# Kernel optimization log

Measured on AMD Instinct MI355X. Metric: run time of the kernel, lower is better.

## Reference

```python
import jax, jax.numpy as jnp
import numpy as np

B, V, F = 16384, 20, 15
H = 256

def setup_inputs() -> dict:
    key = jax.random.key(0)
    ks = jax.random.split(key, 16)
    s = 0.05  # small init scale to keep sigmoids/tanh unsaturated
    return {
        "state": jax.random.normal(ks[0], (B, V, F), jnp.float32),
        "W_ih": jax.random.normal(ks[1], (3 * H, F), jnp.float32) * s,
        "W_hh": jax.random.normal(ks[2], (3 * H, H), jnp.float32) * s,
        "b_ih": jax.random.normal(ks[3], (3 * H,), jnp.float32) * s,
        "b_hh": jax.random.normal(ks[4], (3 * H,), jnp.float32) * s,
        "W1": jax.random.normal(ks[5], (1024, H + F), jnp.float32) * s,
        "b1": jax.random.normal(ks[6], (1024,), jnp.float32) * s,
        "W2": jax.random.normal(ks[7], (1024, 1024), jnp.float32) * s,
        "b2": jax.random.normal(ks[8], (1024,), jnp.float32) * s,
        "W3": jax.random.normal(ks[9], (512, 1024), jnp.float32) * s,
        "b3": jax.random.normal(ks[10], (512,), jnp.float32) * s,
        "W4": jax.random.normal(ks[11], (256, 512), jnp.float32) * s,
        "b4": jax.random.normal(ks[12], (256,), jnp.float32) * s,
        "Wp": jax.random.normal(ks[13], (1, 256), jnp.float32) * s,
        "bp": jax.random.normal(ks[14], (1,), jnp.float32) * s,
    }

def reference(state, W_ih, W_hh, b_ih, b_hh, W1, b1, W2, b2, W3, b3, W4, b4, Wp, bp):
    # state: [B, V, F] -- V vehicles per timestep, F=15 features each.
    # Precompute input-side gate pre-activations for all vehicles: [B, V, 3H]
    xg = jnp.einsum('bvf,gf->bvg', state, W_ih) + b_ih
    h0 = jnp.zeros((state.shape[0], H), state.dtype)

    def gru_step(h, xg_t):  # xg_t: [B, 3H]
        hg = h @ W_hh.T + b_hh  # [B, 3H]
        xr, xz, xn = jnp.split(xg_t, 3, axis=-1)
        hr, hz, hn = jnp.split(hg, 3, axis=-1)
        r = jax.nn.sigmoid(xr + hr)
        z = jax.nn.sigmoid(xz + hz)
        n = jnp.tanh(xn + r * hn)
        return (1.0 - z) * n + z * h, None

    h, _ = jax.lax.scan(gru_step, h0, jnp.swapaxes(xg, 0, 1))  # scan over V
    x = jnp.concatenate([state[:, 0, :], h], axis=-1)  # [B, F+H]
    x = jax.nn.relu(x @ W1.T + b1)
    x = jax.nn.relu(x @ W2.T + b2)
    x = jax.nn.relu(x @ W3.T + b3)
    x = jax.nn.relu(x @ W4.T + b4)
    return jnp.tanh(x @ Wp.T + bp)  # [B, action_dim]
```

## Files before the change

kernel.cpp:

```cpp
#include <hip/hip_runtime.h>


typedef __attribute__((ext_vector_type(8))) __bf16 bf16x8;
typedef __attribute__((ext_vector_type(4))) __bf16 bf16x4;
typedef __attribute__((ext_vector_type(4))) float  floatx4;

#define MFMA16(a, b, c) __builtin_amdgcn_mfma_f32_16x16x32_bf16((a), (b), (c), 0, 0, 0)

#define GL_LDS16(g, l)                                                         \
    __builtin_amdgcn_global_load_lds(                                          \
        (const __attribute__((address_space(1))) void*)(g),                    \
        (__attribute__((address_space(3))) void*)(l), 16, 0, 0)

__device__ __forceinline__ float sigmoid_f(float x) { return 1.f / (1.f + __expf(-x)); }
__device__ __forceinline__ float tanh_f(float x)    { return 1.f - 2.f / (1.f + __expf(2.f * x)); }

#define S0 147456u
#define S1 442368u
#define S2 1490944u
#define S3 2015232u
#define S4 2146304u
#define S5 2154496u
#define S6 2220032u
#define S7 2220544u
#define S8 2221056u

__global__ void prep_kernel(const float* __restrict__ W_ih, const float* __restrict__ W_hh,
                            const float* __restrict__ b_ih, const float* __restrict__ b_hh,
                            const float* __restrict__ W1, const float* __restrict__ W2,
                            const float* __restrict__ W3, const float* __restrict__ W4,
                            __bf16* __restrict__ Wg1, __bf16* __restrict__ W1p,
                            __bf16* __restrict__ W2b, __bf16* __restrict__ W3b,
                            __bf16* __restrict__ W4b, __bf16* __restrict__ Win_n,
                            __bf16* __restrict__ Whh_n, float* __restrict__ bsum,
                            float* __restrict__ bihn, float* __restrict__ bhhn)
{
    for (unsigned i = blockIdx.x * blockDim.x + threadIdx.x; i < S8; i += gridDim.x * blockDim.x) {
        if (i < S0) {
            unsigned g = i / 288u, c = i % 288u;
            float v;
            if (c < 15u)       v = W_ih[g * 15u + c];
            else if (c == 15u) v = b_ih[g] + b_hh[g];
            else if (c < 32u)  v = 0.f;
            else               v = W_hh[g * 256u + (c - 32u)];
            Wg1[i] = (__bf16)v;
        } else if (i < S1) {
            unsigned t = i - S0, o = t / 288u, c = t % 288u;
            float v = (c < 15u) ? W1[o * 271u + c] : ((c < 32u) ? 0.f : W1[o * 271u + (c - 17u)]);
            W1p[t] = (__bf16)v;
        } else if (i < S2) {
            unsigned t = i - S1; W2b[t] = (__bf16)W2[t];
        } else if (i < S3) {
            unsigned t = i - S2; W3b[t] = (__bf16)W3[t];
        } else if (i < S4) {
            unsigned t = i - S3; W4b[t] = (__bf16)W4[t];
        } else if (i < S5) {
            unsigned t = i - S4, j = t / 32u, c = t % 32u;
            float v;
            if (c < 15u)       v = W_ih[(512u + j) * 15u + c];
            else if (c == 15u) v = b_ih[512u + j];
            else               v = 0.f;
            Win_n[t] = (__bf16)v;
        } else if (i < S6) {
            unsigned t = i - S5; Whh_n[t] = (__bf16)W_hh[512u * 256u + t];
        } else if (i < S7) {
            unsigned t = i - S6; bsum[t] = b_ih[t] + b_hh[t];
        } else {
            unsigned t = i - S7;
            if (t < 256u) bihn[t] = b_ih[512u + t];
            else          bhhn[t - 256u] = b_hh[512u + t - 256u];
        }
    }
}

#define HSTRIDE 264
#define HBUF_N  (64 * HSTRIDE)

__global__ __launch_bounds__(1024)
void gru_kernel(const float* __restrict__ state,
                const __bf16* __restrict__ Wg1,  const __bf16* __restrict__ Win_n,
                const __bf16* __restrict__ Whh_n,
                const float* __restrict__ bhhn, __bf16* __restrict__ x0)
{
    __shared__ __bf16 hbuf[2 * HBUF_N];
    __shared__ __bf16 sbuf[2 * 2048];
    __shared__ __bf16 rzbuf[4 * 1024 * 8];

    const int tid  = threadIdx.x;
    const int wave = tid >> 6;
    const int lane = tid & 63;
    const int q    = lane >> 4;
    const int ln   = lane & 15;
    const int b0   = blockIdx.x * 64;

    {
        bf16x8 z = {};
        bf16x8* p = (bf16x8*)hbuf;
        #pragma unroll 3
        for (int i = tid; i < HBUF_N / 8; i += 1024) p[i] = z;
        if (tid < 512) ((bf16x8*)sbuf)[tid] = z;
    }
    const int srow = tid >> 4, sk = tid & 15;

    const floatx4 Bhn = *(const floatx4*)(bhhn + wave * 16 + q * 4);

    const int jr = wave * 16 + ln;
    const __bf16* wr = Wg1   + (size_t)jr * 288 + q * 8;
    const __bf16* wz = Wg1   + (size_t)(256 + jr) * 288 + q * 8;
    const __bf16* wx = Win_n + (size_t)jr * 32  + q * 8;
    const __bf16* wh = Whh_n + (size_t)jr * 256 + q * 8;

    const __bf16* hread  = hbuf + ln * HSTRIDE + q * 8;
    __bf16*       hwrite = hbuf + ln * HSTRIDE + wave * 16 + q * 4;
    const __bf16* sread  = sbuf + ln * 32 + q * 8;
    __bf16*       rzw    = rzbuf + tid * 8;

    if (sk < 15)
        sbuf[srow * 32 + sk] = (__bf16)state[(size_t)(b0 + srow) * 300 + sk];
    if (tid < 128) sbuf[(tid >> 6) * 2048 + (tid & 63) * 32 + 15] = (__bf16)1.0f;
    __syncthreads();

#define GRU_STEP(v, SB)                                                          \
    {                                                                            \
        float snext = 0.f;                                                       \
        if ((v) < 19 && sk < 15)                                                 \
            snext = state[(size_t)(b0 + srow) * 300 + ((v) + 1) * 15 + sk];      \
        _Pragma("unroll 1")                                                      \
        for (int p = 0; p < 2; ++p) {                                            \
            floatx4 acc0[4], acc1[4];                                            \
            const floatx4 zf = {0.f, 0.f, 0.f, 0.f};                             \
            _Pragma("unroll")                                                    \
            for (int nt = 0; nt < 4; nt++) { acc0[nt] = zf; acc1[nt] = zf; }     \
            if (p == 0) {                                                        \
                {                                                                \
                    bf16x8 a0 = *(const bf16x8*)(wr);                            \
                    bf16x8 a1 = *(const bf16x8*)(wz);                            \
                    _Pragma("unroll")                                            \
                    for (int nt = 0; nt < 4; nt++) {                             \
                        bf16x8 b = *(const bf16x8*)(sread + (SB) * 2048 +        \
                                                    nt * 512);                   \
                        acc0[nt] = MFMA16(a0, b, acc0[nt]);                      \
                        acc1[nt] = MFMA16(a1, b, acc1[nt]);                      \
                    }                                                            \
                }                                                                \
                _Pragma("unroll")                                                \
                for (int kk = 0; kk < 8; ++kk) {                                 \
                    bf16x8 a0 = *(const bf16x8*)(wr + 32 + kk * 32);             \
                    bf16x8 a1 = *(const bf16x8*)(wz + 32 + kk * 32);             \
                    _Pragma("unroll")                                            \
                    for (int nt = 0; nt < 4; nt++) {                             \
                        bf16x8 b = *(const bf16x8*)(hread + (SB) * HBUF_N +      \
                                                    nt * (16 * HSTRIDE) +        \
                                                    kk * 32);                    \
                        acc0[nt] = MFMA16(a0, b, acc0[nt]);                      \
                        acc1[nt] = MFMA16(a1, b, acc1[nt]);                      \
                    }                                                            \
                }                                                                \
                _Pragma("unroll")                                                \
                for (int nt = 0; nt < 4; nt++) {                                 \
                    bf16x8 rz;                                                   \
                    _Pragma("unroll")                                            \
                    for (int r = 0; r < 4; r++) {                                \
                        rz[r]     = (__bf16)sigmoid_f(acc0[nt][r]);              \
                        rz[4 + r] = (__bf16)sigmoid_f(acc1[nt][r]);              \
                    }                                                            \
                    *(bf16x8*)(rzw + nt * 8192) = rz;                            \
                }                                                                \
            } else {                                                             \
                {                                                                \
                    bf16x8 a0 = *(const bf16x8*)(wx);                            \
                    _Pragma("unroll")                                            \
                    for (int nt = 0; nt < 4; nt++) {                             \
                        bf16x8 b = *(const bf16x8*)(sread + (SB) * 2048 +        \
                                                    nt * 512);                   \
                        acc0[nt] = MFMA16(a0, b, acc0[nt]);                      \
                    }                                                            \
                }                                                                \
                _Pragma("unroll")                                                \
                for (int kk = 0; kk < 8; ++kk) {                                 \
                    bf16x8 a1 = *(const bf16x8*)(wh + kk * 32);                  \
                    _Pragma("unroll")                                            \
                    for (int nt = 0; nt < 4; nt++) {                             \
                        bf16x8 b = *(const bf16x8*)(hread + (SB) * HBUF_N +      \
                                                    nt * (16 * HSTRIDE) +        \
                                                    kk * 32);                    \
                        acc1[nt] = MFMA16(a1, b, acc1[nt]);                      \
                    }                                                            \
                }                                                                \
                _Pragma("unroll")                                                \
                for (int nt = 0; nt < 4; nt++) {                                 \
                    bf16x8 rz = *(const bf16x8*)(rzw + nt * 8192);               \
                    bf16x4 ho = *(const bf16x4*)(hwrite + (SB) * HBUF_N +        \
                                                 nt * (16 * HSTRIDE));           \
                    bf16x4 hv;                                                   \
                    _Pragma("unroll")                                            \
                    for (int r = 0; r < 4; r++) {                                \
                        float rg = (float)rz[r];                                 \
                        float zg = (float)rz[4 + r];                             \
                        float nn = tanh_f(acc0[nt][r] +                          \
                                          rg * (acc1[nt][r] + Bhn[r]));          \
                        float hnew = (1.f - zg) * nn + zg * (float)ho[r];        \
                        hv[r] = (__bf16)hnew;                                    \
                    }                                                            \
                    *(bf16x4*)(hwrite + (1 - (SB)) * HBUF_N +                    \
                               nt * (16 * HSTRIDE)) = hv;                        \
                }                                                                \
            }                                                                    \
        }                                                                        \
        if ((v) < 19 && sk < 15)                                                 \
            sbuf[(1 - (SB)) * 2048 + srow * 32 + sk] = (__bf16)snext;            \
        __syncthreads();                                                         \
    }

    #pragma unroll 1
    for (int v2 = 0; v2 < 10; ++v2) {
        GRU_STEP(2 * v2,     0)
        GRU_STEP(2 * v2 + 1, 1)
    }
#undef GRU_STEP

    {
        const int row = tid >> 4, p = tid & 15;
        #pragma unroll
        for (int s = 0; s < 2; s++) {
            const int col = p * 8 + s * 128;
            *(bf16x8*)(x0 + (size_t)(b0 + row) * 288 + 32 + col) =
                *(const bf16x8*)(hbuf + row * HSTRIDE + col);
        }
    }
    #pragma unroll
    for (int t = 0; t < 2; t++) {
        int i = tid + t * 1024;
        int row = i >> 5, c = i & 31;
        float s = (c < 15) ? state[(size_t)(b0 + row) * 300 + c] : 0.f;
        x0[(size_t)(b0 + row) * 288 + c] = (__bf16)s;
    }
}

__global__ __launch_bounds__(256)
void gemm_bias_act(const __bf16* __restrict__ A, const __bf16* __restrict__ W,
                   const float* __restrict__ bias, __bf16* __restrict__ C,
                   int N, int K, int relu)
{
    __shared__ __bf16 smem[128 * 136];
    __bf16* At = smem;
    __bf16* Bt = smem + 4096;

    const int tid  = threadIdx.x;
    const int wave = tid >> 6, lane = tid & 63;
    const int q = lane >> 4, ln = lane & 15;
    const int wm = wave >> 1, wn = wave & 1;
    const int arow0 = blockIdx.x * 128;
    const int bcol0 = blockIdx.y * 128;

    float bv[4];
    #pragma unroll
    for (int n = 0; n < 4; n++) bv[n] = bias[bcol0 + wn * 64 + n * 16 + ln];

    floatx4 acc[4][4];
    const floatx4 zf = {0.f, 0.f, 0.f, 0.f};
    #pragma unroll
    for (int m = 0; m < 4; m++)
        #pragma unroll
        for (int n = 0; n < 4; n++) acc[m][n] = zf;

    const int stg_row = wave * 16 + (lane >> 2);
    const int stg_k   = (lane & 3) * 8;
    const int lds_off = wave * 512;

    for (int kt = 0; kt < K; kt += 32) {
        #pragma unroll
        for (int rd = 0; rd < 2; rd++) {
            GL_LDS16(A + (size_t)(arow0 + stg_row + rd * 64) * K + kt + stg_k,
                     At + lds_off + rd * 2048);
            GL_LDS16(W + (size_t)(bcol0 + stg_row + rd * 64) * K + kt + stg_k,
                     Bt + lds_off + rd * 2048);
        }
        __syncthreads();
        bf16x8 af[4], bf[4];
        #pragma unroll
        for (int m = 0; m < 4; m++)
            af[m] = *(const bf16x8*)(At + (wm * 64 + m * 16 + ln) * 32 + q * 8);
        #pragma unroll
        for (int n = 0; n < 4; n++)
            bf[n] = *(const bf16x8*)(Bt + (wn * 64 + n * 16 + ln) * 32 + q * 8);
        #pragma unroll
        for (int n = 0; n < 4; n++)
            #pragma unroll
            for (int m = 0; m < 4; m++)
                acc[m][n] = MFMA16(af[m], bf[n], acc[m][n]);
        __syncthreads();
    }

    #pragma unroll
    for (int m = 0; m < 4; m++)
        #pragma unroll
        for (int n = 0; n < 4; n++)
            #pragma unroll
            for (int r = 0; r < 4; r++) {
                float val = acc[m][n][r] + bv[n];
                if (relu) val = fmaxf(val, 0.f);
                smem[(wm * 64 + m * 16 + q * 4 + r) * 136 + wn * 64 + n * 16 + ln] = (__bf16)val;
            }
    __syncthreads();
    {
        const int row = tid >> 4, seg = tid & 15;
        #pragma unroll
        for (int p = 0; p < 8; p++) {
            const int rr = row + p * 16;
            *(bf16x8*)(C + (size_t)(arow0 + rr) * N + bcol0 + seg * 8) =
                *(const bf16x8*)(smem + rr * 136 + seg * 8);
        }
    }
}

__global__ __launch_bounds__(256)
void head_kernel(const __bf16* __restrict__ x4, const float* __restrict__ Wp,
                 const float* __restrict__ bp, float* __restrict__ out)
{
    const int tid = threadIdx.x;
    const int wave = tid >> 6, lane = tid & 63;
    const int row = blockIdx.x * 64 + wave * 16 + (lane >> 2);
    const int part = lane & 3;
    const __bf16* xp = x4 + (size_t)row * 256 + part * 64;
    const float* wp = Wp + part * 64;
    float sum = 0.f;
    #pragma unroll
    for (int i = 0; i < 8; i++) {
        bf16x8 xv = *(const bf16x8*)(xp + i * 8);
        #pragma unroll
        for (int jj = 0; jj < 8; jj++) sum += (float)xv[jj] * wp[i * 8 + jj];
    }
    sum += __shfl_xor(sum, 1);
    sum += __shfl_xor(sum, 2);
    if (part == 0) out[row] = tanhf(sum + bp[0]);
}

extern "C" void kernel_launch(void* const* d_in, const int* in_sizes, int n_in,
                              void* d_out, int out_size, void* d_ws, size_t ws_size,
                              hipStream_t stream)
{
    const float* state = (const float*)d_in[0];
    const float* W_ih  = (const float*)d_in[1];
    const float* W_hh  = (const float*)d_in[2];
    const float* b_ih  = (const float*)d_in[3];
    const float* b_hh  = (const float*)d_in[4];
    const float* W1    = (const float*)d_in[5];
    const float* b1    = (const float*)d_in[6];
    const float* W2    = (const float*)d_in[7];
    const float* b2    = (const float*)d_in[8];
    const float* W3    = (const float*)d_in[9];
    const float* b3    = (const float*)d_in[10];
    const float* W4    = (const float*)d_in[11];
    const float* b4    = (const float*)d_in[12];
    const float* Wp    = (const float*)d_in[13];
    const float* bp    = (const float*)d_in[14];
    float* out = (float*)d_out;

    char* ws = (char*)d_ws;
    size_t off = 0;
    auto alloc = [&](size_t bytes) -> void* {
        void* p = ws + off;
        off += (bytes + 255) & ~(size_t)255;
        return p;
    };
    __bf16* Wg1   = (__bf16*)alloc(512 * 288 * 2);
    __bf16* W1p   = (__bf16*)alloc(1024 * 288 * 2);
    __bf16* W2b   = (__bf16*)alloc(1024 * 1024 * 2);
    __bf16* W3b   = (__bf16*)alloc(512 * 1024 * 2);
    __bf16* W4b   = (__bf16*)alloc(256 * 512 * 2);
    __bf16* Win_n = (__bf16*)alloc(256 * 32 * 2);
    __bf16* Whh_n = (__bf16*)alloc(256 * 256 * 2);
    float*  bsum  = (float*)alloc(512 * 4);
    float*  bihn  = (float*)alloc(256 * 4);
    float*  bhhn  = (float*)alloc(256 * 4);
    __bf16* x0    = (__bf16*)alloc((size_t)16384 * 288 * 2);
    __bf16* xA    = (__bf16*)alloc((size_t)16384 * 1024 * 2);
    __bf16* xB    = (__bf16*)alloc((size_t)16384 * 1024 * 2);

    prep_kernel<<<2048, 256, 0, stream>>>(W_ih, W_hh, b_ih, b_hh, W1, W2, W3, W4,
                                          Wg1, W1p, W2b, W3b, W4b, Win_n, Whh_n,
                                          bsum, bihn, bhhn);
    gru_kernel<<<256, 1024, 0, stream>>>(state, Wg1, Win_n, Whh_n, bhhn, x0);
    gemm_bias_act<<<dim3(128, 8), 256, 0, stream>>>(x0, W1p, b1, xA, 1024, 288, 1);
    gemm_bias_act<<<dim3(128, 8), 256, 0, stream>>>(xA, W2b, b2, xB, 1024, 1024, 1);
    gemm_bias_act<<<dim3(128, 4), 256, 0, stream>>>(xB, W3b, b3, xA, 512, 1024, 1);
    gemm_bias_act<<<dim3(128, 2), 256, 0, stream>>>(xA, W4b, b4, xB, 256, 512, 1);
    head_kernel<<<256, 256, 0, stream>>>(xB, Wp, bp, out);
}
```

Measured before the change: 463.1 us.

## Remap GRU waves to 64-column by 16-row tiles to reuse h fragments

Each wave in the GRU kernel used to own 16 hidden units across all 64 batch rows, loading a weight fragment once and four h fragments from LDS per k-step. Now waves are split into 4 column groups and 4 row groups, so each wave owns 64 hidden units for 16 batch rows. Per k-step it loads one h fragment from LDS and four weight fragments from global memory/cache. The aim is to cut LDS read traffic and bank pressure, at the cost of more global weight loads per step. The per-wave b_hh bias now comes from memory inside the loop instead of a hoisted register.

After: 1.246 ms. +169.1%, slower.

```diff
diff --git a/kernel.cpp b/kernel.cpp
--- a/kernel.cpp
+++ b/kernel.cpp
@@ -88,6 +88,8 @@
 
     const int tid  = threadIdx.x;
     const int wave = tid >> 6;
+    const int cg   = wave >> 2;
+    const int rg   = wave & 3;
     const int lane = tid & 63;
     const int q    = lane >> 4;
     const int ln   = lane & 15;
@@ -102,18 +104,17 @@
     }
     const int srow = tid >> 4, sk = tid & 15;
 
-    const floatx4 Bhn = *(const floatx4*)(bhhn + wave * 16 + q * 4);
-
-    const int jr = wave * 16 + ln;
-    const __bf16* wr = Wg1   + (size_t)jr * 288 + q * 8;
-    const __bf16* wz = Wg1   + (size_t)(256 + jr) * 288 + q * 8;
-    const __bf16* wx = Win_n + (size_t)jr * 32  + q * 8;
-    const __bf16* wh = Whh_n + (size_t)jr * 256 + q * 8;
-
-    const __bf16* hread  = hbuf + ln * HSTRIDE + q * 8;
-    __bf16*       hwrite = hbuf + ln * HSTRIDE + wave * 16 + q * 4;
-    const __bf16* sread  = sbuf + ln * 32 + q * 8;
-    __bf16*       rzw    = rzbuf + tid * 8;
+    const __bf16* wrB = Wg1   + (size_t)(cg * 64 + ln) * 288 + q * 8;
+    const __bf16* wzB = Wg1   + (size_t)(256 + cg * 64 + ln) * 288 + q * 8;
+    const __bf16* wxB = Win_n + (size_t)(cg * 64 + ln) * 32  + q * 8;
+    const __bf16* whB = Whh_n + (size_t)(cg * 64 + ln) * 256 + q * 8;
+    const float*  bhnB = bhhn + cg * 64 + q * 4;
+
+    const int row = rg * 16 + ln;
+    const __bf16* hread = hbuf + row * HSTRIDE + q * 8;
+    __bf16*       hwrt  = hbuf + row * HSTRIDE + cg * 64 + q * 4;
+    const __bf16* sread = sbuf + row * 32 + q * 8;
+    __bf16*       rzw   = rzbuf + tid * 8;
 
     if (sk < 15)
         sbuf[srow * 32 + sk] = (__bf16)state[(size_t)(b0 + srow) * 300 + sk];
@@ -130,80 +131,78 @@
             floatx4 acc0[4], acc1[4];                                            \
             const floatx4 zf = {0.f, 0.f, 0.f, 0.f};                             \
             _Pragma("unroll")                                                    \
-            for (int nt = 0; nt < 4; nt++) { acc0[nt] = zf; acc1[nt] = zf; }     \
+            for (int jq = 0; jq < 4; jq++) { acc0[jq] = zf; acc1[jq] = zf; }     \
             if (p == 0) {                                                        \
                 {                                                                \
-                    bf16x8 a0 = *(const bf16x8*)(wr);                            \
-                    bf16x8 a1 = *(const bf16x8*)(wz);                            \
-                    _Pragma("unroll")                                            \
-                    for (int nt = 0; nt < 4; nt++) {                             \
-                        bf16x8 b = *(const bf16x8*)(sread + (SB) * 2048 +        \
-                                                    nt * 512);                   \
-                        acc0[nt] = MFMA16(a0, b, acc0[nt]);                      \
-                        acc1[nt] = MFMA16(a1, b, acc1[nt]);                      \
+                    bf16x8 b = *(const bf16x8*)(sread + (SB) * 2048);            \
+                    _Pragma("unroll")                                            \
+                    for (int jq = 0; jq < 4; jq++) {                             \
+                        bf16x8 a0 = *(const bf16x8*)(wrB + jq * 4608);           \
+                        bf16x8 a1 = *(const bf16x8*)(wzB + jq * 4608);           \
+                        acc0[jq] = MFMA16(a0, b, acc0[jq]);                      \
+                        acc1[jq] = MFMA16(a1, b, acc1[jq]);                      \
                     }                                                            \
                 }                                                                \
                 _Pragma("unroll")                                                \
                 for (int kk = 0; kk < 8; ++kk) {                                 \
-                    bf16x8 a0 = *(const bf16x8*)(wr + 32 + kk * 32);             \
-                    bf16x8 a1 = *(const bf16x8*)(wz + 32 + kk * 32);             \
-                    _Pragma("unroll")                                            \
-                    for (int nt = 0; nt < 4; nt++) {                             \
-                        bf16x8 b = *(const bf16x8*)(hread + (SB) * HBUF_N +      \
-                                                    nt * (16 * HSTRIDE) +        \
-                                                    kk * 32);                    \
-                        acc0[nt] = MFMA16(a0, b, acc0[nt]);                      \
-                        acc1[nt] = MFMA16(a1, b, acc1[nt]);                      \
+                    bf16x8 b = *(const bf16x8*)(hread + (SB) * HBUF_N +          \
+                                                kk * 32);                        \
+                    _Pragma("unroll")                                            \
+                    for (int jq = 0; jq < 4; jq++) {                             \
+                        bf16x8 a0 = *(const bf16x8*)(wrB + jq * 4608 + 32 +      \
+                                                     kk * 32);                   \
+                        bf16x8 a1 = *(const bf16x8*)(wzB + jq * 4608 + 32 +      \
+                                                     kk * 32);                   \
+                        acc0[jq] = MFMA16(a0, b, acc0[jq]);                      \
+                        acc1[jq] = MFMA16(a1, b, acc1[jq]);                      \
                     }                                                            \
                 }                                                                \
                 _Pragma("unroll")                                                \
-                for (int nt = 0; nt < 4; nt++) {                                 \
+                for (int jq = 0; jq < 4; jq++) {                                 \
                     bf16x8 rz;                                                   \
                     _Pragma("unroll")                                            \
                     for (int r = 0; r < 4; r++) {                                \
-                        rz[r]     = (__bf16)sigmoid_f(acc0[nt][r]);              \
-                        rz[4 + r] = (__bf16)sigmoid_f(acc1[nt][r]);              \
-                    }                                                            \
-                    *(bf16x8*)(rzw + nt * 8192) = rz;                            \
+                        rz[r]     = (__bf16)sigmoid_f(acc0[jq][r]);              \
+                        rz[4 + r] = (__bf16)sigmoid_f(acc1[jq][r]);              \
+                    }                                                            \
+                    *(bf16x8*)(rzw + jq * 8192) = rz;                            \
                 }                                                                \
             } else {                                                             \
                 {                                                                \
-                    bf16x8 a0 = *(const bf16x8*)(wx);                            \
-                    _Pragma("unroll")                                            \
-                    for (int nt = 0; nt < 4; nt++) {                             \
-                        bf16x8 b = *(const bf16x8*)(sread + (SB) * 2048 +        \
-                                                    nt * 512);                   \
-                        acc0[nt] = MFMA16(a0, b, acc0[nt]);                      \
+                    bf16x8 b = *(const bf16x8*)(sread + (SB) * 2048);            \
+                    _Pragma("unroll")                                            \
+                    for (int jq = 0; jq < 4; jq++) {                             \
+                        bf16x8 a = *(const bf16x8*)(wxB + jq * 512);             \
+                        acc0[jq] = MFMA16(a, b, acc0[jq]);                       \
                     }                                                            \
                 }                                                                \
                 _Pragma("unroll")                                                \
                 for (int kk = 0; kk < 8; ++kk) {                                 \
-                    bf16x8 a1 = *(const bf16x8*)(wh + kk * 32);                  \
-                    _Pragma("unroll")                                            \
-                    for (int nt = 0; nt < 4; nt++) {                             \
-                        bf16x8 b = *(const bf16x8*)(hread + (SB) * HBUF_N +      \
-                                                    nt * (16 * HSTRIDE) +        \
-                                                    kk * 32);                    \
-                        acc1[nt] = MFMA16(a1, b, acc1[nt]);                      \
+                    bf16x8 b = *(const bf16x8*)(hread + (SB) * HBUF_N +          \
+                                                kk * 32);                        \
+                    _Pragma("unroll")                                            \
+                    for (int jq = 0; jq < 4; jq++) {                             \
+                        bf16x8 a = *(const bf16x8*)(whB + jq * 4096 + kk * 32);  \
+                        acc1[jq] = MFMA16(a, b, acc1[jq]);                       \
                     }                                                            \
                 }                                                                \
                 _Pragma("unroll")                                                \
-                for (int nt = 0; nt < 4; nt++) {                                 \
-                    bf16x8 rz = *(const bf16x8*)(rzw + nt * 8192);               \
-                    bf16x4 ho = *(const bf16x4*)(hwrite + (SB) * HBUF_N +        \
-                                                 nt * (16 * HSTRIDE));           \
+                for (int jq = 0; jq < 4; jq++) {                                 \
+                    bf16x8 rz = *(const bf16x8*)(rzw + jq * 8192);               \
+                    floatx4 bh = *(const floatx4*)(bhnB + jq * 16);              \
+                    bf16x4 ho = *(const bf16x4*)(hwrt + (SB) * HBUF_N +          \
+                                                 jq * 16);                       \
                     bf16x4 hv;                                                   \
                     _Pragma("unroll")                                            \
                     for (int r = 0; r < 4; r++) {                                \
-                        float rg = (float)rz[r];                                 \
-                        float zg = (float)rz[4 + r];                             \
-                        float nn = tanh_f(acc0[nt][r] +                          \
-                                          rg * (acc1[nt][r] + Bhn[r]));          \
+                        float rg_ = (float)rz[r];                                \
+                        float zg  = (float)rz[4 + r];                            \
+                        float nn = tanh_f(acc0[jq][r] +                          \
+                                          rg_ * (acc1[jq][r] + bh[r]));          \
                         float hnew = (1.f - zg) * nn + zg * (float)ho[r];        \
                         hv[r] = (__bf16)hnew;                                    \
                     }                                                            \
-                    *(bf16x4*)(hwrite + (1 - (SB)) * HBUF_N +                    \
-                               nt * (16 * HSTRIDE)) = hv;                        \
+                    *(bf16x4*)(hwrt + (1 - (SB)) * HBUF_N + jq * 16) = hv;       \
                 }                                                                \
             }                                                                    \
         }                                                                        \
@@ -220,20 +219,20 @@
 #undef GRU_STEP
 
     {
-        const int row = tid >> 4, p = tid & 15;
+        const int erow = tid >> 4, p = tid & 15;
         #pragma unroll
         for (int s = 0; s < 2; s++) {
             const int col = p * 8 + s * 128;
-            *(bf16x8*)(x0 + (size_t)(b0 + row) * 288 + 32 + col) =
-                *(const bf16x8*)(hbuf + row * HSTRIDE + col);
+            *(bf16x8*)(x0 + (size_t)(b0 + erow) * 288 + 32 + col) =
+                *(const bf16x8*)(hbuf + erow * HSTRIDE + col);
         }
     }
     #pragma unroll
     for (int t = 0; t < 2; t++) {
         int i = tid + t * 1024;
-        int row = i >> 5, c = i & 31;
-        float s = (c < 15) ? state[(size_t)(b0 + row) * 300 + c] : 0.f;
-        x0[(size_t)(b0 + row) * 288 + c] = (__bf16)s;
+        int erow = i >> 5, c = i & 31;
+        float s = (c < 15) ? state[(size_t)(b0 + erow) * 300 + c] : 0.f;
+        x0[(size_t)(b0 + erow) * 288 + c] = (__bf16)s;
     }
 }
 
```
